# Performance work log

Measured on AMD Instinct MI355X. Metric: run time of the kernel, lower is better.

## Reference

```python
import jax, jax.numpy as jnp
import numpy as np

E, C, D, F = 8, 2048, 2048, 8192  # experts, capacity/expert, d_model, d_ff

def setup_inputs() -> dict:
    key = jax.random.key(0)
    ks = jax.random.split(key, 5)
    s_in = 1.0 / np.sqrt(D)
    s_h = 1.0 / np.sqrt(F)
    return {
        "inputs": jax.random.normal(ks[0], (1, E * C, D), dtype=jnp.float32),
        "w1": jax.random.normal(ks[1], (E, D, F), dtype=jnp.float32) * s_in,
        "b1": jax.random.normal(ks[2], (E, F), dtype=jnp.float32) * 0.01,
        "w2": jax.random.normal(ks[3], (E, F, D), dtype=jnp.float32) * s_h,
        "b2": jax.random.normal(ks[4], (E, D), dtype=jnp.float32) * 0.01,
    }

def reference(inputs, w1, b1, w2, b2):
    # inputs: [G, E*C, D]; chunk along dim=1 == reshape to [G, E, C, D]
    G, T, d = inputs.shape
    x = inputs.reshape(G, E, T // E, d)
    # grouped FFN: per-expert Linear -> GELU(exact, torch default) -> Linear
    h = jnp.einsum('gecd,edf->gecf', x, w1) + b1[None, :, None, :]
    h = jax.nn.gelu(h, approximate=False)
    y = jnp.einsum('gecf,efd->gecd', h, w2) + b2[None, :, None, :]
    # torch.cat(expert_outputs, dim=1) == reshape back
    return y.reshape(G, T, d)
```

## Files before the change

### kernel.cpp

```cpp
#include <hip/hip_runtime.h>
#include <hip/hip_bf16.h>


#define E_ 8
#define C_ 2048
#define D_ 2048
#define F_ 8192

typedef short bf16x8 __attribute__((ext_vector_type(8)));
typedef float f32x4  __attribute__((ext_vector_type(4)));

__device__ inline unsigned short f2bf(float f) {
    unsigned u = __float_as_uint(f);
    u += 0x7fffu + ((u >> 16) & 1u);
    return (unsigned short)(u >> 16);
}

__device__ inline float gelu_fast(float x) {
    float z = 0.7978845608028654f * (x + 0.044715f * x * x * x);
    float e = __expf(-2.0f * fabsf(z));
    float t = (1.0f - e) / (1.0f + e);
    t = copysignf(t, z);
    return 0.5f * x * (1.0f + t);
}

__device__ inline void gload_lds16(const void* g, void* l) {
    __builtin_amdgcn_global_load_lds(
        (const __attribute__((address_space(1))) void*)g,
        (__attribute__((address_space(3))) void*)l, 16, 0, 0);
}

__global__ __launch_bounds__(256) void cvt_kernel(
    const float* __restrict__ in, unsigned short* __restrict__ out, long n4)
{
    long i = (long)blockIdx.x * 256 + threadIdx.x;
    if (i >= n4) return;
    float4 v = ((const float4*)in)[i];
    union { unsigned short u[4]; uint2 q; } r;
    r.u[0] = f2bf(v.x); r.u[1] = f2bf(v.y); r.u[2] = f2bf(v.z); r.u[3] = f2bf(v.w);
    ((uint2*)out)[i] = r.q;
}

__global__ __launch_bounds__(256) void transpose_cvt(
    const float* __restrict__ in, unsigned short* __restrict__ out,
    int R, int Cc, int RT, int CT)
{
    __shared__ float lds[64][65];
    int bx = blockIdx.x;
    int e  = bx / (RT * CT);
    int rem = bx % (RT * CT);
    int rt = rem / CT, ct = rem % CT;
    const float* ine = in + (long)e * R * Cc;
    unsigned short* oute = out + (long)e * R * Cc;
    long r0 = (long)rt * 64, c0 = (long)ct * 64;
    int t = threadIdx.x;

    int lr = t >> 4, lc = t & 15;
#pragma unroll
    for (int ii = 0; ii < 4; ++ii) {
        int r = lr + ii * 16;
        float4 v = *(const float4*)(ine + (r0 + r) * Cc + c0 + lc * 4);
        lds[r][lc * 4 + 0] = v.x; lds[r][lc * 4 + 1] = v.y;
        lds[r][lc * 4 + 2] = v.z; lds[r][lc * 4 + 3] = v.w;
    }
    __syncthreads();

    int nl = t >> 3, kv = t & 7;
#pragma unroll
    for (int ii = 0; ii < 2; ++ii) {
        int n = nl + ii * 32;
        union { unsigned short u[8]; uint4 q; } r;
#pragma unroll
        for (int j = 0; j < 8; ++j) r.u[j] = f2bf(lds[kv * 8 + j][n]);
        *(uint4*)(oute + (c0 + n) * R + r0 + kv * 8) = r.q;
    }
}

#define REG_A0 0
#define REG_A1 16384
#define REG_B0 32768
#define REG_B1 49152
#define SLOT_B 65536

#define MFMA16(d, a, b) d = __builtin_amdgcn_mfma_f32_16x16x32_bf16(a, b, d, 0, 0, 0)

template <bool GELU, bool OUT_BF16>
__global__ __launch_bounds__(512, 2) void gemm8p(
    const unsigned short* __restrict__ A,
    const unsigned short* __restrict__ Bt,
    const float* __restrict__ bias,
    void* __restrict__ Cout,
    int M, int N, int K,
    long strideAe, long strideBe, long strideCe, int biasStride)
{
    extern __shared__ char ldsb[];

    constexpr int BM = 256, BN = 256, BK = 64, GRP = 4;
    int MT = M / BM, NT = N / BN;
    int per = MT * NT;
    int nwg = gridDim.x;
    int bid = blockIdx.x;
    int tile = (nwg % 8 == 0) ? (bid & 7) * (nwg >> 3) + (bid >> 3) : bid;
    int e = tile / per, s = tile % per;
    int ng  = s / (MT * GRP);
    int r2  = s % (MT * GRP);
    int mt  = r2 >> 2;
    int nt  = ng * GRP + (r2 & 3);

    const unsigned short* Ae = A  + (long)e * strideAe + (long)mt * BM * K;
    const unsigned short* Be = Bt + (long)e * strideBe + (long)nt * BN * K;

    int tid = threadIdx.x, lane = tid & 63, wid = tid >> 6;
    int wr = wid >> 2, wc = wid & 3;

    int g0 = wid * 128 + lane, g1 = g0 + 64;
    long sOff0, sOff1; int sDst0, sDst1;
    { int row = g0 >> 2, col = g0 & 3, sw = col ^ ((row >> 1) & 3);
      sOff0 = (long)row * K + sw * 8; sDst0 = g0 * 16; }
    { int row = g1 >> 2, col = g1 & 3, sw = col ^ ((row >> 1) & 3);
      sOff1 = (long)row * K + sw * 8; sDst1 = g1 * 16; }

    auto stage_region = [&](const unsigned short* base, int ktile, int kreg, int dstByte) {
        long k0 = (long)ktile * BK + kreg * 32;
        gload_lds16(base + sOff0 + k0, ldsb + dstByte + sDst0);
        gload_lds16(base + sOff1 + k0, ldsb + dstByte + sDst1);
    };

    f32x4 acc[8][4] = {};
    int KT = K / BK;

    int rbaseA = wr * 128 + (lane & 15);
    int rbaseB = wc * 64  + (lane & 15);
    int kq = lane >> 4;
    int baseA = rbaseA * 64 + ((kq ^ ((rbaseA >> 1) & 3)) << 4);
    int baseB = REG_B0 + rbaseB * 64 + ((kq ^ ((rbaseB >> 1) & 3)) << 4);

    stage_region(Ae, 0, 0, REG_A0);
    stage_region(Be, 0, 0, REG_B0);
    stage_region(Ae, 0, 1, REG_A1);
    stage_region(Be, 0, 1, REG_B1);
    stage_region(Ae, 1, 0, SLOT_B + REG_A0);
    stage_region(Be, 1, 0, SLOT_B + REG_B0);
    stage_region(Ae, 1, 1, SLOT_B + REG_A1);

    bf16x8 a[8][2], b[4][2];

    for (int T = 0; T < KT; ++T) {
        int so = (T & 1) * SLOT_B;
        const char* pA = ldsb + so + baseA;
        const char* pB = ldsb + so + baseB;

        if (T == KT - 1) asm volatile("s_waitcnt vmcnt(0)" ::: "memory");
        else             asm volatile("s_waitcnt vmcnt(6)" ::: "memory");
        __builtin_amdgcn_sched_barrier(0);
        __builtin_amdgcn_s_barrier();
        __builtin_amdgcn_sched_barrier(0);

        #pragma unroll
        for (int n = 0; n < 2; ++n) {
            b[n][0] = *(const bf16x8*)(pB + n * 1024);
            b[n][1] = *(const bf16x8*)(pB + 16384 + n * 1024);
        }
        #pragma unroll
        for (int m = 0; m < 4; ++m) {
            a[m][0] = *(const bf16x8*)(pA + m * 1024);
            a[m][1] = *(const bf16x8*)(pA + 16384 + m * 1024);
        }
        if (T + 1 < KT) stage_region(Be, T + 1, 1, (so ^ SLOT_B) + REG_B1);
        __builtin_amdgcn_s_barrier();
        __builtin_amdgcn_s_setprio(1);
        #pragma unroll
        for (int m = 0; m < 4; ++m)
            #pragma unroll
            for (int n = 0; n < 2; ++n) {
                MFMA16(acc[m][n], a[m][0], b[n][0]);
                MFMA16(acc[m][n], a[m][1], b[n][1]);
            }
        __builtin_amdgcn_s_setprio(0);
        __builtin_amdgcn_s_barrier();

        #pragma unroll
        for (int n = 2; n < 4; ++n) {
            b[n][0] = *(const bf16x8*)(pB + n * 1024);
            b[n][1] = *(const bf16x8*)(pB + 16384 + n * 1024);
        }
        __builtin_amdgcn_s_barrier();
        __builtin_amdgcn_s_setprio(1);
        #pragma unroll
        for (int m = 0; m < 4; ++m)
            #pragma unroll
            for (int n = 2; n < 4; ++n) {
                MFMA16(acc[m][n], a[m][0], b[n][0]);
                MFMA16(acc[m][n], a[m][1], b[n][1]);
            }
        __builtin_amdgcn_s_setprio(0);
        __builtin_amdgcn_s_barrier();

        #pragma unroll
        for (int m = 4; m < 8; ++m) {
            a[m][0] = *(const bf16x8*)(pA + m * 1024);
            a[m][1] = *(const bf16x8*)(pA + 16384 + m * 1024);
        }
        if (T + 2 < KT) stage_region(Be, T + 2, 0, so + REG_B0);
        __builtin_amdgcn_s_barrier();
        __builtin_amdgcn_s_setprio(1);
        #pragma unroll
        for (int m = 4; m < 8; ++m)
            #pragma unroll
            for (int n = 0; n < 2; ++n) {
                MFMA16(acc[m][n], a[m][0], b[n][0]);
                MFMA16(acc[m][n], a[m][1], b[n][1]);
            }
        __builtin_amdgcn_s_setprio(0);
        __builtin_amdgcn_s_barrier();

        if (T + 2 < KT) {
            stage_region(Ae, T + 2, 0, so + REG_A0);
            stage_region(Ae, T + 2, 1, so + REG_A1);
        }
        __builtin_amdgcn_s_barrier();
        __builtin_amdgcn_s_setprio(1);
        #pragma unroll
        for (int m = 4; m < 8; ++m)
            #pragma unroll
            for (int n = 2; n < 4; ++n) {
                MFMA16(acc[m][n], a[m][0], b[n][0]);
                MFMA16(acc[m][n], a[m][1], b[n][1]);
            }
        __builtin_amdgcn_s_setprio(0);
        __builtin_amdgcn_s_barrier();
    }

    const float* be = bias + (long)e * biasStride + nt * BN;
    long cBase = (long)e * strideCe + ((long)mt * BM) * N + (long)nt * BN;
#pragma unroll
    for (int m = 0; m < 8; ++m) {
#pragma unroll
        for (int n = 0; n < 4; ++n) {
            int col = wc * 64 + n * 16 + (lane & 15);
            float bv = be[col];
#pragma unroll
            for (int j = 0; j < 4; ++j) {
                int row = wr * 128 + m * 16 + (lane >> 4) * 4 + j;
                float v = acc[m][n][j] + bv;
                if (GELU) v = gelu_fast(v);
                long idx = cBase + (long)row * N + col;
                if (OUT_BF16) ((unsigned short*)Cout)[idx] = f2bf(v);
                else          ((float*)Cout)[idx] = v;
            }
        }
    }
}

extern "C" void kernel_launch(void* const* d_in, const int* in_sizes, int n_in,
                              void* d_out, int out_size, void* d_ws, size_t ws_size,
                              hipStream_t stream)
{
    const float* x  = (const float*)d_in[0];
    const float* w1 = (const float*)d_in[1];
    const float* b1 = (const float*)d_in[2];
    const float* w2 = (const float*)d_in[3];
    const float* b2 = (const float*)d_in[4];
    float* out = (float*)d_out;

    (void)hipFuncSetAttribute((const void*)gemm8p<true, true>,
                              hipFuncAttributeMaxDynamicSharedMemorySize, 131072);
    (void)hipFuncSetAttribute((const void*)gemm8p<false, false>,
                              hipFuncAttributeMaxDynamicSharedMemorySize, 131072);

    const long CD = (long)C_ * D_;
    const long DF = (long)D_ * F_;
    const long CF = (long)C_ * F_;
    const long perExpertElems = CD + 2 * DF + CF;
    long ceMax = (long)(ws_size / ((size_t)perExpertElems * 2));
    int CE = (int)(ceMax < 1 ? 1 : (ceMax > E_ ? E_ : ceMax));

    unsigned short* xb  = (unsigned short*)d_ws;
    unsigned short* w1t = xb  + (long)CE * CD;
    unsigned short* w2t = w1t + (long)CE * DF;
    unsigned short* h   = w2t + (long)CE * DF;

    for (int e0 = 0; e0 < E_; e0 += CE) {
        int ce = (E_ - e0) < CE ? (E_ - e0) : CE;

        long n4 = (long)ce * CD / 4;
        cvt_kernel<<<(int)((n4 + 255) / 256), 256, 0, stream>>>(
            x + (long)e0 * CD, xb, n4);

        transpose_cvt<<<ce * (D_ / 64) * (F_ / 64), 256, 0, stream>>>(
            w1 + (long)e0 * DF, w1t, D_, F_, D_ / 64, F_ / 64);

        transpose_cvt<<<ce * (F_ / 64) * (D_ / 64), 256, 0, stream>>>(
            w2 + (long)e0 * DF, w2t, F_, D_, F_ / 64, D_ / 64);

        gemm8p<true, true><<<ce * (C_ / 256) * (F_ / 256), 512, 131072, stream>>>(
            xb, w1t, b1 + (long)e0 * F_, (void*)h,
            C_, F_, D_, CD, DF, CF, F_);

        gemm8p<false, false><<<ce * (C_ / 256) * (D_ / 256), 512, 131072, stream>>>(
            h, w2t, b2 + (long)e0 * D_, (void*)(out + (long)e0 * CD),
            C_, D_, F_, CF, DF, CD, D_);
    }
}
```

Measured before the change: 1.483 ms.

## Restructure GEMM main loop into two half-K phases with fewer barriers

```diff
diff --git a/kernel.cpp b/kernel.cpp
--- a/kernel.cpp
+++ b/kernel.cpp
@@ -83,9 +83,12 @@
 #define SLOT_B 65536
 
 #define MFMA16(d, a, b) d = __builtin_amdgcn_mfma_f32_16x16x32_bf16(a, b, d, 0, 0, 0)
+#define CHECKPOINT8() do { \
+    asm volatile("s_waitcnt vmcnt(8)" ::: "memory"); \
+    __builtin_amdgcn_s_barrier(); } while (0)
 
 template <bool GELU, bool OUT_BF16>
-__global__ __launch_bounds__(512, 2) void gemm8p(
+__global__ __launch_bounds__(512, 2) void gemm2p(
     const unsigned short* __restrict__ A,
     const unsigned short* __restrict__ Bt,
     const float* __restrict__ bias,
@@ -141,95 +144,47 @@
     stage_region(Be, 0, 1, REG_B1);
     stage_region(Ae, 1, 0, SLOT_B + REG_A0);
     stage_region(Be, 1, 0, SLOT_B + REG_B0);
-    stage_region(Ae, 1, 1, SLOT_B + REG_A1);
-
-    bf16x8 a[8][2], b[4][2];
+    CHECKPOINT8();
 
     for (int T = 0; T < KT; ++T) {
         int so = (T & 1) * SLOT_B;
         const char* pA = ldsb + so + baseA;
         const char* pB = ldsb + so + baseB;
-
-        if (T == KT - 1) asm volatile("s_waitcnt vmcnt(0)" ::: "memory");
-        else             asm volatile("s_waitcnt vmcnt(6)" ::: "memory");
-        __builtin_amdgcn_sched_barrier(0);
-        __builtin_amdgcn_s_barrier();
-        __builtin_amdgcn_sched_barrier(0);
-
-        #pragma unroll
-        for (int n = 0; n < 2; ++n) {
-            b[n][0] = *(const bf16x8*)(pB + n * 1024);
-            b[n][1] = *(const bf16x8*)(pB + 16384 + n * 1024);
-        }
-        #pragma unroll
-        for (int m = 0; m < 4; ++m) {
-            a[m][0] = *(const bf16x8*)(pA + m * 1024);
-            a[m][1] = *(const bf16x8*)(pA + 16384 + m * 1024);
-        }
-        if (T + 1 < KT) stage_region(Be, T + 1, 1, (so ^ SLOT_B) + REG_B1);
-        __builtin_amdgcn_s_barrier();
-        __builtin_amdgcn_s_setprio(1);
-        #pragma unroll
-        for (int m = 0; m < 4; ++m)
-            #pragma unroll
-            for (int n = 0; n < 2; ++n) {
-                MFMA16(acc[m][n], a[m][0], b[n][0]);
-                MFMA16(acc[m][n], a[m][1], b[n][1]);
-            }
-        __builtin_amdgcn_s_setprio(0);
-        __builtin_amdgcn_s_barrier();
-
-        #pragma unroll
-        for (int n = 2; n < 4; ++n) {
-            b[n][0] = *(const bf16x8*)(pB + n * 1024);
-            b[n][1] = *(const bf16x8*)(pB + 16384 + n * 1024);
-        }
-        __builtin_amdgcn_s_barrier();
-        __builtin_amdgcn_s_setprio(1);
-        #pragma unroll
-        for (int m = 0; m < 4; ++m)
-            #pragma unroll
-            for (int n = 2; n < 4; ++n) {
-                MFMA16(acc[m][n], a[m][0], b[n][0]);
-                MFMA16(acc[m][n], a[m][1], b[n][1]);
-            }
-        __builtin_amdgcn_s_setprio(0);
-        __builtin_amdgcn_s_barrier();
-
-        #pragma unroll
-        for (int m = 4; m < 8; ++m) {
-            a[m][0] = *(const bf16x8*)(pA + m * 1024);
-            a[m][1] = *(const bf16x8*)(pA + 16384 + m * 1024);
-        }
-        if (T + 2 < KT) stage_region(Be, T + 2, 0, so + REG_B0);
-        __builtin_amdgcn_s_barrier();
-        __builtin_amdgcn_s_setprio(1);
-        #pragma unroll
-        for (int m = 4; m < 8; ++m)
-            #pragma unroll
-            for (int n = 0; n < 2; ++n) {
-                MFMA16(acc[m][n], a[m][0], b[n][0]);
-                MFMA16(acc[m][n], a[m][1], b[n][1]);
-            }
-        __builtin_amdgcn_s_setprio(0);
-        __builtin_amdgcn_s_barrier();
-
-        if (T + 2 < KT) {
-            stage_region(Ae, T + 2, 0, so + REG_A0);
-            stage_region(Ae, T + 2, 1, so + REG_A1);
-        }
-        __builtin_amdgcn_s_barrier();
-        __builtin_amdgcn_s_setprio(1);
-        #pragma unroll
-        for (int m = 4; m < 8; ++m)
-            #pragma unroll
-            for (int n = 2; n < 4; ++n) {
-                MFMA16(acc[m][n], a[m][0], b[n][0]);
-                MFMA16(acc[m][n], a[m][1], b[n][1]);
-            }
-        __builtin_amdgcn_s_setprio(0);
-        __builtin_amdgcn_s_barrier();
-    }
+        int k1 = (T + 1 < KT) ? T + 1 : KT - 1;
+        int k2 = (T + 2 < KT) ? T + 2 : KT - 1;
+        int so1 = (k1 & 1) * SLOT_B;
+        int so2 = (k2 & 1) * SLOT_B;
+
+        bf16x8 a0[8], b0[4];
+#pragma unroll
+        for (int n = 0; n < 4; ++n) b0[n] = *(const bf16x8*)(pB + n * 1024);
+#pragma unroll
+        for (int m = 0; m < 8; ++m) a0[m] = *(const bf16x8*)(pA + m * 1024);
+        stage_region(Ae, k1, 1, so1 + REG_A1);
+        stage_region(Be, k1, 1, so1 + REG_B1);
+#pragma unroll
+        for (int m = 0; m < 8; ++m)
+#pragma unroll
+            for (int n = 0; n < 4; ++n)
+                MFMA16(acc[m][n], a0[m], b0[n]);
+        CHECKPOINT8();
+
+        bf16x8 a1[8], b1[4];
+#pragma unroll
+        for (int n = 0; n < 4; ++n) b1[n] = *(const bf16x8*)(pB + 16384 + n * 1024);
+#pragma unroll
+        for (int m = 0; m < 8; ++m) a1[m] = *(const bf16x8*)(pA + 16384 + m * 1024);
+        stage_region(Ae, k2, 0, so2 + REG_A0);
+        stage_region(Be, k2, 0, so2 + REG_B0);
+#pragma unroll
+        for (int m = 0; m < 8; ++m)
+#pragma unroll
+            for (int n = 0; n < 4; ++n)
+                MFMA16(acc[m][n], a1[m], b1[n]);
+        CHECKPOINT8();
+    }
+
+    asm volatile("s_waitcnt vmcnt(0)" ::: "memory");
 
     const float* be = bias + (long)e * biasStride + nt * BN;
     long cBase = (long)e * strideCe + ((long)mt * BM) * N + (long)nt * BN;
@@ -263,9 +218,9 @@
     const float* b2 = (const float*)d_in[4];
     float* out = (float*)d_out;
 
-    (void)hipFuncSetAttribute((const void*)gemm8p<true, true>,
+    (void)hipFuncSetAttribute((const void*)gemm2p<true, true>,
                               hipFuncAttributeMaxDynamicSharedMemorySize, 131072);
-    (void)hipFuncSetAttribute((const void*)gemm8p<false, false>,
+    (void)hipFuncSetAttribute((const void*)gemm2p<false, false>,
                               hipFuncAttributeMaxDynamicSharedMemorySize, 131072);
 
     const long CD = (long)C_ * D_;
@@ -293,11 +248,11 @@
         transpose_cvt<<<ce * (F_ / 64) * (D_ / 64), 256, 0, stream>>>(
             w2 + (long)e0 * DF, w2t, F_, D_, F_ / 64, D_ / 64);
 
-        gemm8p<true, true><<<ce * (C_ / 256) * (F_ / 256), 512, 131072, stream>>>(
+        gemm2p<true, true><<<ce * (C_ / 256) * (F_ / 256), 512, 131072, stream>>>(
             xb, w1t, b1 + (long)e0 * F_, (void*)h,
             C_, F_, D_, CD, DF, CF, F_);
 
-        gemm8p<false, false><<<ce * (C_ / 256) * (D_ / 256), 512, 131072, stream>>>(
+        gemm2p<false, false><<<ce * (C_ / 256) * (D_ / 256), 512, 131072, stream>>>(
             h, w2t, b2 + (long)e0 * D_, (void*)(out + (long)e0 * CD),
             C_, D_, F_, CF, DF, CD, D_);
     }
```

After: 1.359 ms (median of 3 runs). 1.09x faster.
